# Kernel optimization log

Measured on AMD Instinct MI355X. Metric: run time of the kernel, lower is better.

The kernel has to match this reference:

```python
import jax, jax.numpy as jnp
import numpy as np

K, N, M = 65536, 4096, 64  # observations, basis centers, features


def setup_inputs() -> dict:
    key = jax.random.key(0)
    k1, k2, k3, k4 = jax.random.split(key, 4)
    x = jax.random.normal(k1, (K, M), dtype=jnp.float32)
    x_basis = jax.random.normal(k2, (N, M), dtype=jnp.float32)
    w = jax.random.normal(k3, (1, N), dtype=jnp.float32) / np.sqrt(N)
    b = jax.random.normal(k4, (1,), dtype=jnp.float32)
    return {"x": x, "x_basis": x_basis, "w": w, "b": b}


def reference(x, x_basis, w, b):
    # pairwise squared distances ||x_i - c_j||^2, [K, N]
    x2 = jnp.sum(x * x, axis=1, keepdims=True)          # [K, 1]
    c2 = jnp.sum(x_basis * x_basis, axis=1)             # [N]
    sq = x2 + c2[None, :] - 2.0 * (x @ x_basis.T)       # [K, N]
    phi = jnp.exp(-sq)                                  # gaussian RBF
    return jax.nn.sigmoid(phi @ w.T + b)                # [K, 1]
```

## Files before the change

### kernel.cpp

```cpp
#include <hip/hip_runtime.h>


#define KOBS 65536
#define NCENT 4096
#define MFEAT 64
#define BR 64
#define BN 128
#define NCHUNK (NCENT / BN)
#define KBLK (KOBS / BR)

#define SCALE_A 2.8853900817779268f
#define QS      1.4426950408889634f
#define TSKIP   -60.0f

typedef __attribute__((ext_vector_type(8))) short short8;
typedef __attribute__((ext_vector_type(4))) float float4v;
typedef __attribute__((ext_vector_type(2))) float float2v;

#if __has_builtin(__builtin_amdgcn_exp2f)
#define EXP2F(x) __builtin_amdgcn_exp2f(x)
#else
#define EXP2F(x) exp2f(x)
#endif

static __device__ inline short f2bf(float f) {
    unsigned int u = __float_as_uint(f);
    unsigned int r = (u + 0x7fffu + ((u >> 16) & 1u)) >> 16;
    return (short)r;
}

__global__ __launch_bounds__(256) void rbf_prep(
    const float* __restrict__ xb, const float* __restrict__ w,
    short* __restrict__ cb, float2v* __restrict__ hc2w) {
    const int bid = blockIdx.x;
    const int tid = threadIdx.x;
    if (bid < 128) {
        const int o    = bid * 256 + tid;
        const int tile = o >> 7;
        const int r    = o & 127;
        const int p    = r >> 6;
        const int g    = (r >> 4) & 3;
        const int mm   = r & 15;
        const int row  = tile * 16 + mm;
        const int k0   = p * 32 + g * 8;
        float4v v0 = *(const float4v*)(xb + row * MFEAT + k0);
        float4v v1 = *(const float4v*)(xb + row * MFEAT + k0 + 4);
        short8 oct;
        #pragma unroll
        for (int j = 0; j < 4; ++j) { oct[j] = f2bf(v0[j]); oct[j + 4] = f2bf(v1[j]); }
        *(short8*)(cb + o * 8) = oct;
    } else {
        const int row  = (bid - 128) * 4 + (tid >> 6);
        const int lane = tid & 63;
        float v = xb[row * MFEAT + lane];
        float s = v * v;
        #pragma unroll
        for (int off = 32; off > 0; off >>= 1) s += __shfl_xor(s, off, 64);
        if (lane == 0) {
            float2v hw = {-QS * s, w[row]};
            hc2w[row] = hw;
        }
    }
}

__global__ __launch_bounds__(256, 4) void rbf_main(
    const float* __restrict__ x, const short* __restrict__ cb,
    const float2v* __restrict__ hc2w, const float* __restrict__ bptr,
    float* __restrict__ out) {
    __shared__ float x2s[BR];
    __shared__ float red[4 * BR];

    const int tid  = threadIdx.x;
    const int wave = tid >> 6;
    const int lane = tid & 63;
    const int m    = lane & 15;
    const int g    = lane >> 4;
    const int r0   = (int)blockIdx.x * BR;

    short8 af[4][2];
    float  ssr[4];
    #pragma unroll
    for (int rg = 0; rg < 4; ++rg) {
        const float* xr = x + (r0 + rg * 16 + m) * MFEAT + g * 8;
        float4v a0 = *(const float4v*)(xr);
        float4v a1 = *(const float4v*)(xr + 4);
        float4v a2 = *(const float4v*)(xr + 32);
        float4v a3 = *(const float4v*)(xr + 36);
        float ss = 0.0f;
        #pragma unroll
        for (int i = 0; i < 4; ++i) {
            af[rg][0][i]     = f2bf(SCALE_A * a0[i]);  ss = fmaf(a0[i], a0[i], ss);
            af[rg][0][i + 4] = f2bf(SCALE_A * a1[i]);  ss = fmaf(a1[i], a1[i], ss);
            af[rg][1][i]     = f2bf(SCALE_A * a2[i]);  ss = fmaf(a2[i], a2[i], ss);
            af[rg][1][i + 4] = f2bf(SCALE_A * a3[i]);  ss = fmaf(a3[i], a3[i], ss);
        }
        ss += __shfl_xor(ss, 16, 64);
        ss += __shfl_xor(ss, 32, 64);
        ssr[rg] = ss;
    }
    if (g == 0) {
        #pragma unroll
        for (int rg = 0; rg < 4; ++rg) x2s[rg * 16 + m] = ssr[rg];
    }
    __syncthreads();

    float4v p4v[4];
    #pragma unroll
    for (int rg = 0; rg < 4; ++rg)
        #pragma unroll
        for (int i = 0; i < 4; ++i) p4v[rg][i] = -QS * x2s[rg * 16 + g * 4 + i];

    float accw[4][4];
    #pragma unroll
    for (int rg = 0; rg < 4; ++rg)
        #pragma unroll
        for (int i = 0; i < 4; ++i) accw[rg][i] = 0.0f;

    const char* cbb = (const char*)cb + wave * 4096 + lane * 16;
    const float2v* hwp = hc2w + wave * 32 + m;

    short8  pb0[2][2], pb1[2][2];
    float2v phw[2][2];

    #define LOADT(c, tt, s) do {                                              \
        pb0[s][tt] = *(const short8*)(cbb + (c) * 16384 + (tt) * 2048);       \
        pb1[s][tt] = *(const short8*)(cbb + (c) * 16384 + (tt) * 2048 + 1024);\
        float2v hw_ = hwp[(c) * 128 + (tt) * 16];                             \
        hw_.x = TSKIP - hw_.x;                                                \
        phw[s][tt] = hw_;                                                     \
    } while (0)

    LOADT(0, 0, 0);
    LOADT(0, 1, 0);

    #pragma unroll 2
    for (int c = 0; c < NCHUNK; ++c) {
        const int cur = c & 1, nxt = cur ^ 1;
        if (c + 1 < NCHUNK) {
            LOADT(c + 1, 0, nxt);
            LOADT(c + 1, 1, nxt);
        }
        #pragma unroll
        for (int tt2 = 0; tt2 < 2; ++tt2) {
            short8 b0 = pb0[cur][tt2];
            short8 b1 = pb1[cur][tt2];
            float  tq = phw[cur][tt2].x;
            float  wv = phw[cur][tt2].y;
            #pragma unroll
            for (int rp = 0; rp < 2; ++rp) {
                const int rg0 = rp * 2, rg1 = rp * 2 + 1;
                float4v a0 = __builtin_amdgcn_mfma_f32_16x16x32_bf16(
                    af[rg0][0], b0, p4v[rg0], 0, 0, 0);
                a0 = __builtin_amdgcn_mfma_f32_16x16x32_bf16(
                    af[rg0][1], b1, a0, 0, 0, 0);
                float4v a1 = __builtin_amdgcn_mfma_f32_16x16x32_bf16(
                    af[rg1][0], b0, p4v[rg1], 0, 0, 0);
                a1 = __builtin_amdgcn_mfma_f32_16x16x32_bf16(
                    af[rg1][1], b1, a1, 0, 0, 0);
                float mx = fmaxf(
                    fmaxf(fmaxf(a0[0], a0[1]), fmaxf(a0[2], a0[3])),
                    fmaxf(fmaxf(a1[0], a1[1]), fmaxf(a1[2], a1[3])));
                if (__any(mx > tq)) {
                    float q = TSKIP - tq;
                    #pragma unroll
                    for (int i = 0; i < 4; ++i) {
                        accw[rg0][i] = fmaf(wv, EXP2F(a0[i] + q), accw[rg0][i]);
                        accw[rg1][i] = fmaf(wv, EXP2F(a1[i] + q), accw[rg1][i]);
                    }
                }
            }
        }
    }

    #pragma unroll
    for (int rg = 0; rg < 4; ++rg)
        #pragma unroll
        for (int i = 0; i < 4; ++i) {
            float v = accw[rg][i];
            v += __shfl_xor(v, 1, 64);
            v += __shfl_xor(v, 2, 64);
            v += __shfl_xor(v, 4, 64);
            v += __shfl_xor(v, 8, 64);
            accw[rg][i] = v;
        }
    if (m == 0) {
        #pragma unroll
        for (int rg = 0; rg < 4; ++rg)
            #pragma unroll
            for (int i = 0; i < 4; ++i)
                red[wave * BR + rg * 16 + g * 4 + i] = accw[rg][i];
    }
    __syncthreads();
    if (tid < BR) {
        float z = red[tid] + red[BR + tid] + red[2 * BR + tid] + red[3 * BR + tid]
                + bptr[0];
        out[r0 + tid] = 1.0f / (1.0f + EXP2F(-QS * z));
    }
}

extern "C" void kernel_launch(void* const* d_in, const int* in_sizes, int n_in,
                              void* d_out, int out_size, void* d_ws, size_t ws_size,
                              hipStream_t stream) {
    const float* x  = (const float*)d_in[0];
    const float* xb = (const float*)d_in[1];
    const float* w  = (const float*)d_in[2];
    const float* b  = (const float*)d_in[3];
    float* out = (float*)d_out;

    short*   cb   = (short*)d_ws;
    float2v* hc2w = (float2v*)((char*)d_ws + NCENT * MFEAT * 2);

    rbf_prep<<<128 + NCENT / 4, 256, 0, stream>>>(xb, w, cb, hc2w);
    rbf_main<<<KBLK, 256, 0, stream>>>(x, cb, hc2w, b, out);
}
```

Before: 106.4 us.

## Switch RBF distance GEMM to FP8 32x32x64 scaled MFMA with LDS atomics

Both operands of the distance GEMM (observations and basis centers) are now quantised to FP8 instead of BF16, and each wave issues 32x32x64 scaled MFMAs in place of 16x16x32 BF16 tiles. This halves the basis bytes loaded and cuts the number of MFMA instructions. The per-lane weighted accumulation with a final shuffle reduction is replaced by shared-memory atomicAdds on the rare non-skipped entries, and s_setprio is raised around the MFMAs. It risks accuracy loss from FP8 rounding of values scaled by about 2.9 inside an exponential, plus LDS atomic contention when many entries pass the threshold.

Result: faster. 90.32 us (-15.1%).

```diff
diff --git a/kernel.cpp b/kernel.cpp
--- a/kernel.cpp
+++ b/kernel.cpp
@@ -13,9 +13,10 @@
 #define QS      1.4426950408889634f
 #define TSKIP   -60.0f
 
-typedef __attribute__((ext_vector_type(8))) short short8;
-typedef __attribute__((ext_vector_type(4))) float float4v;
-typedef __attribute__((ext_vector_type(2))) float float2v;
+typedef __attribute__((ext_vector_type(4)))  float float4v;
+typedef __attribute__((ext_vector_type(2)))  float float2v;
+typedef __attribute__((ext_vector_type(16))) float float16v;
+typedef __attribute__((ext_vector_type(8)))  int   int8v;
 
 #if __has_builtin(__builtin_amdgcn_exp2f)
 #define EXP2F(x) __builtin_amdgcn_exp2f(x)
@@ -23,32 +24,30 @@
 #define EXP2F(x) exp2f(x)
 #endif
 
-static __device__ inline short f2bf(float f) {
-    unsigned int u = __float_as_uint(f);
-    unsigned int r = (u + 0x7fffu + ((u >> 16) & 1u)) >> 16;
-    return (short)r;
-}
-
 __global__ __launch_bounds__(256) void rbf_prep(
     const float* __restrict__ xb, const float* __restrict__ w,
-    short* __restrict__ cb, float2v* __restrict__ hc2w) {
+    char* __restrict__ cb, float2v* __restrict__ hc2w) {
     const int bid = blockIdx.x;
     const int tid = threadIdx.x;
     if (bid < 128) {
-        const int o    = bid * 256 + tid;
-        const int tile = o >> 7;
-        const int r    = o & 127;
-        const int p    = r >> 6;
-        const int g    = (r >> 4) & 3;
-        const int mm   = r & 15;
-        const int row  = tile * 16 + mm;
-        const int k0   = p * 32 + g * 8;
-        float4v v0 = *(const float4v*)(xb + row * MFEAT + k0);
-        float4v v1 = *(const float4v*)(xb + row * MFEAT + k0 + 4);
-        short8 oct;
-        #pragma unroll
-        for (int j = 0; j < 4; ++j) { oct[j] = f2bf(v0[j]); oct[j + 4] = f2bf(v1[j]); }
-        *(short8*)(cb + o * 8) = oct;
+        const int o      = bid * 256 + tid;
+        const int col    = o >> 3;
+        const int joct   = o & 7;
+        const int c      = col >> 7;
+        const int w4     = (col >> 5) & 3;
+        const int lanelo = col & 31;
+        const int l      = lanelo + (joct >> 2) * 32;
+        const int j0     = (joct & 3) * 8;
+        const float* src = xb + col * MFEAT + joct * 8;
+        float4v v0 = *(const float4v*)(src);
+        float4v v1 = *(const float4v*)(src + 4);
+        int lo = __builtin_amdgcn_cvt_pk_fp8_f32(v0[0], v0[1], 0, false);
+        lo     = __builtin_amdgcn_cvt_pk_fp8_f32(v0[2], v0[3], lo, true);
+        int hi = __builtin_amdgcn_cvt_pk_fp8_f32(v1[0], v1[1], 0, false);
+        hi     = __builtin_amdgcn_cvt_pk_fp8_f32(v1[2], v1[3], hi, true);
+        unsigned long long pk = (unsigned long long)(unsigned)lo |
+                                ((unsigned long long)(unsigned)hi << 32);
+        *(unsigned long long*)(cb + (size_t)((c * 4 + w4) * 64 + l) * 32 + j0) = pk;
     } else {
         const int row  = (bid - 128) * 4 + (tid >> 6);
         const int lane = tid & 63;
@@ -64,136 +63,110 @@
 }
 
 __global__ __launch_bounds__(256, 4) void rbf_main(
-    const float* __restrict__ x, const short* __restrict__ cb,
+    const float* __restrict__ x, const char* __restrict__ cb,
     const float2v* __restrict__ hc2w, const float* __restrict__ bptr,
     float* __restrict__ out) {
     __shared__ float x2s[BR];
-    __shared__ float red[4 * BR];
+    __shared__ float zl[BR];
 
     const int tid  = threadIdx.x;
     const int wave = tid >> 6;
     const int lane = tid & 63;
-    const int m    = lane & 15;
-    const int g    = lane >> 4;
+    const int ll   = lane & 31;
+    const int lh   = lane >> 5;
     const int r0   = (int)blockIdx.x * BR;
 
-    short8 af[4][2];
-    float  ssr[4];
+    if (tid < BR) zl[tid] = 0.0f;
+
+    int8v af[2];
+    float ssv[2];
     #pragma unroll
-    for (int rg = 0; rg < 4; ++rg) {
-        const float* xr = x + (r0 + rg * 16 + m) * MFEAT + g * 8;
-        float4v a0 = *(const float4v*)(xr);
-        float4v a1 = *(const float4v*)(xr + 4);
-        float4v a2 = *(const float4v*)(xr + 32);
-        float4v a3 = *(const float4v*)(xr + 36);
+    for (int t = 0; t < 2; ++t) {
+        const float* xr = x + (size_t)(r0 + t * 32 + ll) * MFEAT + lh * 32;
+        int8v a;
         float ss = 0.0f;
         #pragma unroll
-        for (int i = 0; i < 4; ++i) {
-            af[rg][0][i]     = f2bf(SCALE_A * a0[i]);  ss = fmaf(a0[i], a0[i], ss);
-            af[rg][0][i + 4] = f2bf(SCALE_A * a1[i]);  ss = fmaf(a1[i], a1[i], ss);
-            af[rg][1][i]     = f2bf(SCALE_A * a2[i]);  ss = fmaf(a2[i], a2[i], ss);
-            af[rg][1][i + 4] = f2bf(SCALE_A * a3[i]);  ss = fmaf(a3[i], a3[i], ss);
+        for (int rg = 0; rg < 8; ++rg) {
+            float4v v = *(const float4v*)(xr + rg * 4);
+            ss = fmaf(v[0], v[0], ss); ss = fmaf(v[1], v[1], ss);
+            ss = fmaf(v[2], v[2], ss); ss = fmaf(v[3], v[3], ss);
+            int pk = __builtin_amdgcn_cvt_pk_fp8_f32(
+                SCALE_A * v[0], SCALE_A * v[1], 0, false);
+            pk = __builtin_amdgcn_cvt_pk_fp8_f32(
+                SCALE_A * v[2], SCALE_A * v[3], pk, true);
+            a[rg] = pk;
         }
-        ss += __shfl_xor(ss, 16, 64);
         ss += __shfl_xor(ss, 32, 64);
-        ssr[rg] = ss;
+        af[t]  = a;
+        ssv[t] = ss;
     }
-    if (g == 0) {
-        #pragma unroll
-        for (int rg = 0; rg < 4; ++rg) x2s[rg * 16 + m] = ssr[rg];
+    if (wave == 0 && lh == 0) {
+        x2s[ll]      = ssv[0];
+        x2s[32 + ll] = ssv[1];
     }
     __syncthreads();
 
-    float4v p4v[4];
+    const int rb = 4 * lh;
+    float16v p0, p1;
     #pragma unroll
-    for (int rg = 0; rg < 4; ++rg)
-        #pragma unroll
-        for (int i = 0; i < 4; ++i) p4v[rg][i] = -QS * x2s[rg * 16 + g * 4 + i];
+    for (int i = 0; i < 16; ++i) {
+        const int ri = rb + (i & 3) + 8 * (i >> 2);
+        p0[i] = -QS * x2s[ri];
+        p1[i] = -QS * x2s[32 + ri];
+    }
 
-    float accw[4][4];
-    #pragma unroll
-    for (int rg = 0; rg < 4; ++rg)
-        #pragma unroll
-        for (int i = 0; i < 4; ++i) accw[rg][i] = 0.0f;
+    const char* cbb = cb + wave * 2048 + lane * 32;
+    const float2v* hwp = hc2w + wave * 32 + ll;
 
-    const char* cbb = (const char*)cb + wave * 4096 + lane * 16;
-    const float2v* hwp = hc2w + wave * 32 + m;
+    int8v   pb[2];
+    float2v phw[2];
 
-    short8  pb0[2][2], pb1[2][2];
-    float2v phw[2][2];
-
-    #define LOADT(c, tt, s) do {                                              \
-        pb0[s][tt] = *(const short8*)(cbb + (c) * 16384 + (tt) * 2048);       \
-        pb1[s][tt] = *(const short8*)(cbb + (c) * 16384 + (tt) * 2048 + 1024);\
-        float2v hw_ = hwp[(c) * 128 + (tt) * 16];                             \
-        hw_.x = TSKIP - hw_.x;                                                \
-        phw[s][tt] = hw_;                                                     \
+    #define LOADB(c, s) do {                               \
+        pb[s] = *(const int8v*)(cbb + (c) * 8192);         \
+        float2v hw_ = hwp[(c) * 128];                      \
+        hw_.x = TSKIP - hw_.x;                             \
+        phw[s] = hw_;                                      \
     } while (0)
 
-    LOADT(0, 0, 0);
-    LOADT(0, 1, 0);
+    LOADB(0, 0);
 
     #pragma unroll 2
     for (int c = 0; c < NCHUNK; ++c) {
         const int cur = c & 1, nxt = cur ^ 1;
-        if (c + 1 < NCHUNK) {
-            LOADT(c + 1, 0, nxt);
-            LOADT(c + 1, 1, nxt);
-        }
+        if (c + 1 < NCHUNK) LOADB(c + 1, nxt);
+        __builtin_amdgcn_s_setprio(1);
+        float16v a0 = __builtin_amdgcn_mfma_scale_f32_32x32x64_f8f6f4(
+            af[0], pb[cur], p0, 0, 0, 0, 0x7f7f7f7f, 0, 0x7f7f7f7f);
+        float16v a1 = __builtin_amdgcn_mfma_scale_f32_32x32x64_f8f6f4(
+            af[1], pb[cur], p1, 0, 0, 0, 0x7f7f7f7f, 0, 0x7f7f7f7f);
+        __builtin_amdgcn_s_setprio(0);
+        const float tq = phw[cur].x;
+        const float wv = phw[cur].y;
         #pragma unroll
-        for (int tt2 = 0; tt2 < 2; ++tt2) {
-            short8 b0 = pb0[cur][tt2];
-            short8 b1 = pb1[cur][tt2];
-            float  tq = phw[cur][tt2].x;
-            float  wv = phw[cur][tt2].y;
-            #pragma unroll
-            for (int rp = 0; rp < 2; ++rp) {
-                const int rg0 = rp * 2, rg1 = rp * 2 + 1;
-                float4v a0 = __builtin_amdgcn_mfma_f32_16x16x32_bf16(
-                    af[rg0][0], b0, p4v[rg0], 0, 0, 0);
-                a0 = __builtin_amdgcn_mfma_f32_16x16x32_bf16(
-                    af[rg0][1], b1, a0, 0, 0, 0);
-                float4v a1 = __builtin_amdgcn_mfma_f32_16x16x32_bf16(
-                    af[rg1][0], b0, p4v[rg1], 0, 0, 0);
-                a1 = __builtin_amdgcn_mfma_f32_16x16x32_bf16(
-                    af[rg1][1], b1, a1, 0, 0, 0);
-                float mx = fmaxf(
-                    fmaxf(fmaxf(a0[0], a0[1]), fmaxf(a0[2], a0[3])),
-                    fmaxf(fmaxf(a1[0], a1[1]), fmaxf(a1[2], a1[3])));
-                if (__any(mx > tq)) {
-                    float q = TSKIP - tq;
+        for (int t = 0; t < 2; ++t) {
+            float16v av = t ? a1 : a0;
+            float m0 = fmaxf(fmaxf(av[0],  av[1]),  av[2]);
+            float m1 = fmaxf(fmaxf(av[3],  av[4]),  av[5]);
+            float m2 = fmaxf(fmaxf(av[6],  av[7]),  av[8]);
+            float m3 = fmaxf(fmaxf(av[9],  av[10]), av[11]);
+            float m4 = fmaxf(fmaxf(av[12], av[13]), av[14]);
+            float mx = fmaxf(fmaxf(fmaxf(m0, m1), m2),
+                             fmaxf(fmaxf(m3, m4), av[15]));
+            if (__any(mx > tq)) {
+                const float q = TSKIP - tq;
+                if (mx > tq) {
                     #pragma unroll
-                    for (int i = 0; i < 4; ++i) {
-                        accw[rg0][i] = fmaf(wv, EXP2F(a0[i] + q), accw[rg0][i]);
-                        accw[rg1][i] = fmaf(wv, EXP2F(a1[i] + q), accw[rg1][i]);
-                    }
+                    for (int i = 0; i < 16; ++i)
+                        atomicAdd(&zl[t * 32 + rb + (i & 3) + 8 * (i >> 2)],
+                                  wv * EXP2F(av[i] + q));
                 }
             }
         }
     }
 
-    #pragma unroll
-    for (int rg = 0; rg < 4; ++rg)
-        #pragma unroll
-        for (int i = 0; i < 4; ++i) {
-            float v = accw[rg][i];
-            v += __shfl_xor(v, 1, 64);
-            v += __shfl_xor(v, 2, 64);
-            v += __shfl_xor(v, 4, 64);
-            v += __shfl_xor(v, 8, 64);
-            accw[rg][i] = v;
-        }
-    if (m == 0) {
-        #pragma unroll
-        for (int rg = 0; rg < 4; ++rg)
-            #pragma unroll
-            for (int i = 0; i < 4; ++i)
-                red[wave * BR + rg * 16 + g * 4 + i] = accw[rg][i];
-    }
     __syncthreads();
     if (tid < BR) {
-        float z = red[tid] + red[BR + tid] + red[2 * BR + tid] + red[3 * BR + tid]
-                + bptr[0];
+        float z = zl[tid] + bptr[0];
         out[r0 + tid] = 1.0f / (1.0f + EXP2F(-QS * z));
     }
 }
@@ -207,8 +180,8 @@
     const float* b  = (const float*)d_in[3];
     float* out = (float*)d_out;
 
-    short*   cb   = (short*)d_ws;
-    float2v* hc2w = (float2v*)((char*)d_ws + NCENT * MFEAT * 2);
+    char*    cb   = (char*)d_ws;
+    float2v* hc2w = (float2v*)((char*)d_ws + NCENT * MFEAT);
 
     rbf_prep<<<128 + NCENT / 4, 256, 0, stream>>>(xb, w, cb, hc2w);
     rbf_main<<<KBLK, 256, 0, stream>>>(x, cb, hc2w, b, out);
```
